# Kernel tuning notes

Measured on AMD Instinct MI355X. Metric: run time of the kernel, lower is better.

## Reference

```python
import jax, jax.numpy as jnp
import numpy as np

H = 256

def setup_inputs() -> dict:
    key = jax.random.key(0)
    ks = jax.random.split(key, 9)
    s = 1.0 / np.sqrt(H)
    x = jax.random.normal(ks[0], (8, 2048, H), dtype=jnp.float32)
    Wq = jax.random.uniform(ks[1], (H, H), jnp.float32, -s, s)
    bq = jax.random.uniform(ks[2], (H,), jnp.float32, -s, s)
    Wk = jax.random.uniform(ks[3], (H, H), jnp.float32, -s, s)
    bk = jax.random.uniform(ks[4], (H,), jnp.float32, -s, s)
    Wv = jax.random.uniform(ks[5], (H, H), jnp.float32, -s, s)
    bv = jax.random.uniform(ks[6], (H,), jnp.float32, -s, s)
    Ww = jax.random.uniform(ks[7], (H, 1), jnp.float32, -s, s)
    bw = jax.random.uniform(ks[8], (1,), jnp.float32, -s, s)
    return {"x": x, "Wq": Wq, "bq": bq, "Wk": Wk, "bk": bk,
            "Wv": Wv, "bv": bv, "Ww": Ww, "bw": bw}

def reference(x, Wq, bq, Wk, bk, Wv, bv, Ww, bw):
    # x: (B, N, H) — cross-asset attention over N assets
    q = x @ Wq + bq
    k = x @ Wk + bk
    v = x @ Wv + bv
    scale = 1.0 / jnp.sqrt(jnp.asarray(q.shape[-1], q.dtype))
    beta = jnp.einsum('bnd,bmd->bnm', q, k) * scale  # (B, N, N)
    beta = jax.nn.softmax(beta, axis=-1)
    # original: sum(value[:,None] * beta[...,None], dim=2) == beta @ v
    out = jnp.einsum('bnm,bmd->bnd', beta, v)
    final_scores = (out @ Ww + bw)[..., 0]  # (B, N)
    return final_scores
```

## Files before the change

kernel.cpp:

```cpp
#include <hip/hip_runtime.h>

#define H 256
#define NB 2048
#define BATCH 8
#define NSPLIT 8
#define KSPAN (NB / NSPLIT)
#define NITER (KSPAN / 64)

typedef unsigned short u16;
using bf16x8 = __attribute__((ext_vector_type(8))) __bf16;
using f32x4  = __attribute__((ext_vector_type(4))) float;

typedef const __attribute__((address_space(1))) void gv_t;
typedef __attribute__((address_space(3))) void lv_t;

__device__ __forceinline__ void gl_lds16(const void* g, void* l) {
    __builtin_amdgcn_global_load_lds((gv_t*)g, (lv_t*)l, 16, 0, 0);
}

#define MFMA(a, b, c) __builtin_amdgcn_mfma_f32_16x16x32_bf16(a, b, c, 0, 0, 0)

__device__ __forceinline__ u16 f2bf(float f) {
    union { float f; unsigned u; } v; v.f = f;
    unsigned r = v.u + 0x7fffu + ((v.u >> 16) & 1u);
    return (u16)(r >> 16);
}

__device__ __forceinline__ bf16x8 cvt8(const float* p) {
    float4 f0 = *(const float4*)p;
    float4 f1 = *(const float4*)(p + 4);
    union { bf16x8 v; u16 u[8]; } r;
    r.u[0] = f2bf(f0.x); r.u[1] = f2bf(f0.y); r.u[2] = f2bf(f0.z); r.u[3] = f2bf(f0.w);
    r.u[4] = f2bf(f1.x); r.u[5] = f2bf(f1.y); r.u[6] = f2bf(f1.z); r.u[7] = f2bf(f1.w);
    return r.v;
}

__global__ __launch_bounds__(256) void prep_kernel(
        const float* __restrict__ Wq, const float* __restrict__ Wk,
        const float* __restrict__ Wv, const float* __restrict__ Ww,
        const float* __restrict__ bq, const float* __restrict__ bv,
        u16* __restrict__ aTb, float* __restrict__ wvw,
        float* __restrict__ kbv, float* __restrict__ ccp, int* __restrict__ cnt) {
    __shared__ u16 bt[16384];
    int id = blockIdx.x, t = threadIdx.x;

    if (id < 256) {
        int f = id;
        if (id == 0 && t < 64) cnt[t] = 0;
        float p = Wv[f * H + t] * Ww[t];
        float r = Wk[f * H + t] * bq[t];
        float c = (id == 0) ? bv[t] * Ww[t] : 0.f;
        for (int o = 32; o; o >>= 1) {
            p += __shfl_xor(p, o); r += __shfl_xor(r, o); c += __shfl_xor(c, o);
        }
        __shared__ float redp[4], redr[4], redc[4];
        int w = t >> 6, lane = t & 63;
        if (lane == 0) { redp[w] = p; redr[w] = r; redc[w] = c; }
        __syncthreads();
        if (t == 0) {
            wvw[f] = redp[0] + redp[1] + redp[2] + redp[3];
            kbv[f] = redr[0] + redr[1] + redr[2] + redr[3];
            if (f == 0) ccp[0] = redc[0] + redc[1] + redc[2] + redc[3];
        }
        return;
    }

    int gid = id - 256;
    int mb = (gid >> 2) * 128, nb = (gid & 3) * 64;
    int w = t >> 6, lane = t & 63, l15 = lane & 15, quad = lane >> 4;

    {
        const float* src = Wq + (nb + w * 16 + l15) * H + quad * 8;
        #pragma unroll
        for (int ks = 0; ks < 8; ++ks)
            *(bf16x8*)(bt + (w * 8 + ks) * 512 + lane * 8) = cvt8(src + ks * 32);
    }

    bf16x8 a[2][8];
    #pragma unroll
    for (int mi = 0; mi < 2; ++mi) {
        const float* ab = Wk + (mb + w * 32 + mi * 16 + l15) * H + quad * 8;
        #pragma unroll
        for (int ks = 0; ks < 8; ++ks) a[mi][ks] = cvt8(ab + ks * 32);
    }
    __syncthreads();

    f32x4 acc[2][4] = {};
    #pragma unroll
    for (int ks = 0; ks < 8; ++ks)
        #pragma unroll
        for (int tt = 0; tt < 4; ++tt) {
            bf16x8 b = *(const bf16x8*)(bt + ((tt * 8 + ks) * 64 + lane) * 8);
            acc[0][tt] = MFMA(a[0][ks], b, acc[0][tt]);
            acc[1][tt] = MFMA(a[1][ks], b, acc[1][tt]);
        }

    #pragma unroll
    for (int mi = 0; mi < 2; ++mi) {
        int m = mb + w * 32 + mi * 16 + quad * 4;
        #pragma unroll
        for (int tt = 0; tt < 4; ++tt) {
            int n = nb + tt * 16 + l15;
            #pragma unroll
            for (int r2 = 0; r2 < 4; ++r2)
                aTb[(m + r2) * H + n] = f2bf(acc[mi][tt][r2] * 0.0625f);
        }
    }
}

__global__ __launch_bounds__(256) void xt_kernel(
        const float* __restrict__ x, const u16* __restrict__ aTb,
        const float* __restrict__ wvw, const float* __restrict__ kbv,
        const float* __restrict__ ccp,
        u16* __restrict__ xbf, float2* __restrict__ uee, u16* __restrict__ Tbf) {
    int id = blockIdx.x, tid = threadIdx.x;
    int w = tid >> 6, lane = tid & 63, l15 = lane & 15, quad = lane >> 4;
    int rb = id * 32;

    bf16x8 a[2][8];
    float s[2] = {0.f, 0.f}, d[2] = {0.f, 0.f};
    #pragma unroll
    for (int ks = 0; ks < 8; ++ks) {
        const float* wp = wvw + ks * 32 + quad * 8;
        const float* kp = kbv + ks * 32 + quad * 8;
        float4 w0 = *(const float4*)wp, w1 = *(const float4*)(wp + 4);
        float4 k0 = *(const float4*)kp, k1 = *(const float4*)(kp + 4);
        #pragma unroll
        for (int mi = 0; mi < 2; ++mi) {
            const float* xr = x + (size_t)(rb + mi * 16 + l15) * H + ks * 32 + quad * 8;
            float4 f0 = *(const float4*)xr;
            float4 f1 = *(const float4*)(xr + 4);
            union { bf16x8 v; u16 u[8]; } r;
            r.u[0] = f2bf(f0.x); r.u[1] = f2bf(f0.y); r.u[2] = f2bf(f0.z); r.u[3] = f2bf(f0.w);
            r.u[4] = f2bf(f1.x); r.u[5] = f2bf(f1.y); r.u[6] = f2bf(f1.z); r.u[7] = f2bf(f1.w);
            a[mi][ks] = r.v;
            s[mi] += f0.x * w0.x + f0.y * w0.y + f0.z * w0.z + f0.w * w0.w
                   + f1.x * w1.x + f1.y * w1.y + f1.z * w1.z + f1.w * w1.w;
            d[mi] += f0.x * k0.x + f0.y * k0.y + f0.z * k0.z + f0.w * k0.w
                   + f1.x * k1.x + f1.y * k1.y + f1.z * k1.z + f1.w * k1.w;
        }
    }

    if (w == 0) {
        #pragma unroll
        for (int mi = 0; mi < 2; ++mi) {
            u16* xo = xbf + (size_t)(rb + mi * 16 + l15) * H + quad * 8;
            #pragma unroll
            for (int ks = 0; ks < 8; ++ks)
                *(bf16x8*)(xo + ks * 32) = a[mi][ks];
        }
        float cc = ccp[0];
        #pragma unroll
        for (int mi = 0; mi < 2; ++mi) {
            float ss = s[mi] + __shfl_xor(s[mi], 16); ss += __shfl_xor(ss, 32);
            float dd = d[mi] + __shfl_xor(d[mi], 16); dd += __shfl_xor(dd, 32);
            if (quad == 0) {
                float e = __expf(dd * 0.0625f);
                uee[rb + mi * 16 + l15] = make_float2(e * (ss + cc), e);
            }
        }
    }

    #pragma unroll 1
    for (int t = 0; t < 4; ++t) {
        int n = (w * 4 + t) * 16 + l15;
        const u16* bb = aTb + n * H + quad * 8;
        bf16x8 bfr[8];
        #pragma unroll
        for (int ks = 0; ks < 8; ++ks) bfr[ks] = *(const bf16x8*)(bb + ks * 32);
        f32x4 acc0 = {}, acc1 = {};
        #pragma unroll
        for (int ks = 0; ks < 8; ++ks) {
            acc0 = MFMA(a[0][ks], bfr[ks], acc0);
            acc1 = MFMA(a[1][ks], bfr[ks], acc1);
        }
        #pragma unroll
        for (int r2 = 0; r2 < 4; ++r2) {
            Tbf[(size_t)(rb + quad * 4 + r2) * H + n]      = f2bf(acc0[r2]);
            Tbf[(size_t)(rb + 16 + quad * 4 + r2) * H + n] = f2bf(acc1[r2]);
        }
    }
}

__global__ __launch_bounds__(256, 2) void attn_kernel(
        const u16* __restrict__ T, const u16* __restrict__ xbf,
        const float2* __restrict__ uee, const float* __restrict__ bw,
        float* __restrict__ pnum, float* __restrict__ pden,
        int* __restrict__ cnt, float* __restrict__ out) {
    __shared__ u16 kt[32768];
    __shared__ int lastf;
    int tid = threadIdx.x;
    int id = blockIdx.x;
    int b = id & 7, rest = id >> 3;
    int qc = rest & 7, sp = rest >> 3;
    int w = tid >> 6, lane = tid & 63, l15 = lane & 15, quad = lane >> 4;
    int qb = qc * 256;

    bf16x8 aq[4][8];
    {
        const u16* qbase = T + (size_t)(b * NB + qb + w * 64 + l15) * H + quad * 8;
        #pragma unroll
        for (int mi = 0; mi < 4; ++mi)
            #pragma unroll
            for (int ks = 0; ks < 8; ++ks)
                aq[mi][ks] = *(const bf16x8*)(qbase + mi * 16 * H + ks * 32);
    }

    const u16* xb = xbf + (size_t)b * NB * H;
    const float2* uep = uee + (size_t)b * NB;
    const int kb0 = sp * KSPAN;

    const u16* gsrc = xb + (size_t)(kb0 + w * 16 + l15) * H + quad * 8;
    #pragma unroll
    for (int j = 0; j < 8; ++j)
        gl_lds16(gsrc + j * 32, kt + (w * 8 + j) * 512);
    __syncthreads();

    float ls[4][4] = {}, as_[4][4] = {};

    #pragma unroll 1
    for (int h = 0; h < NITER; ++h) {
        const u16* ktc = kt + (h & 1) * 16384;
        if (h + 1 < NITER) {
            u16* dst = kt + ((h & 1) ^ 1) * 16384;
            const u16* g2 = gsrc + (size_t)(h + 1) * 64 * H;
            #pragma unroll
            for (int j = 0; j < 8; ++j)
                gl_lds16(g2 + j * 32, dst + (w * 8 + j) * 512);
        }
        int kb64 = kb0 + h * 64;
        float2 uv[4];
        #pragma unroll
        for (int t = 0; t < 4; ++t) uv[t] = uep[kb64 + t * 16 + l15];

        #pragma unroll
        for (int t = 0; t < 4; ++t) {
            f32x4 acc[4] = {};
            __builtin_amdgcn_s_setprio(1);
            #pragma unroll
            for (int ks = 0; ks < 8; ++ks) {
                bf16x8 bfr = *(const bf16x8*)(ktc + ((t * 8 + ks) * 64 + lane) * 8);
                acc[0] = MFMA(aq[0][ks], bfr, acc[0]);
                acc[1] = MFMA(aq[1][ks], bfr, acc[1]);
                acc[2] = MFMA(aq[2][ks], bfr, acc[2]);
                acc[3] = MFMA(aq[3][ks], bfr, acc[3]);
            }
            __builtin_amdgcn_s_setprio(0);
            #pragma unroll
            for (int mi = 0; mi < 4; ++mi)
                #pragma unroll
                for (int r = 0; r < 4; ++r) {
                    float p = __expf(acc[mi][r]);
                    as_[mi][r] += p * uv[t].x;
                    ls[mi][r]  += p * uv[t].y;
                }
        }
        __syncthreads();
    }

    #pragma unroll
    for (int mi = 0; mi < 4; ++mi)
        #pragma unroll
        for (int r = 0; r < 4; ++r)
            for (int o = 1; o < 16; o <<= 1) {
                ls[mi][r]  += __shfl_xor(ls[mi][r], o);
                as_[mi][r] += __shfl_xor(as_[mi][r], o);
            }

    if (l15 == 0) {
        size_t base = (size_t)(sp * BATCH + b) * NB + qb + w * 64 + quad * 4;
        #pragma unroll
        for (int mi = 0; mi < 4; ++mi)
            #pragma unroll
            for (int r = 0; r < 4; ++r) {
                pnum[base + mi * 16 + r] = as_[mi][r];
                pden[base + mi * 16 + r] = ls[mi][r];
            }
    }

    __syncthreads();
    if (tid == 0) {
        __threadfence();
        int old = atomicAdd(cnt + (b * 8 + qc), 1);
        lastf = (old == NSPLIT - 1) ? 1 : 0;
    }
    __syncthreads();
    if (lastf) {
        __threadfence();
        int row = qb + tid;
        float num = 0.f, den = 0.f;
        #pragma unroll
        for (int s2 = 0; s2 < NSPLIT; ++s2) {
            num += pnum[(size_t)(s2 * BATCH + b) * NB + row];
            den += pden[(size_t)(s2 * BATCH + b) * NB + row];
        }
        out[(size_t)b * NB + row] = num / den + bw[0];
    }
}

extern "C" void kernel_launch(void* const* d_in, const int* in_sizes, int n_in,
                              void* d_out, int out_size, void* d_ws, size_t ws_size,
                              hipStream_t stream) {
    (void)in_sizes; (void)n_in; (void)out_size; (void)ws_size;
    const float* x  = (const float*)d_in[0];
    const float* Wq = (const float*)d_in[1];
    const float* bq = (const float*)d_in[2];
    const float* Wk = (const float*)d_in[3];
    const float* bk = (const float*)d_in[4];  (void)bk;
    const float* Wv = (const float*)d_in[5];
    const float* bv = (const float*)d_in[6];
    const float* Ww = (const float*)d_in[7];
    const float* bw = (const float*)d_in[8];
    float* out = (float*)d_out;

    u16* xbf = (u16*)d_ws;
    u16* Tbf = xbf + 4194304;
    u16* aTb = Tbf + 4194304;
    float* wvw = (float*)(aTb + 65536);
    float* kbv = wvw + 256;
    float* ccp = kbv + 256;
    float2* uee = (float2*)(ccp + 4);
    float* pnum = (float*)(uee + 16384);
    float* pden = pnum + NSPLIT * BATCH * NB;
    int* cnt = (int*)(pden + NSPLIT * BATCH * NB);

    hipLaunchKernelGGL(prep_kernel, dim3(264), dim3(256), 0, stream,
                       Wq, Wk, Wv, Ww, bq, bv, aTb, wvw, kbv, ccp, cnt);
    hipLaunchKernelGGL(xt_kernel, dim3(512), dim3(256), 0, stream,
                       x, aTb, wvw, kbv, ccp, xbf, uee, Tbf);
    hipLaunchKernelGGL(attn_kernel, dim3(8 * 8 * NSPLIT), dim3(256), 0, stream,
                       Tbf, xbf, uee, bw, pnum, pden, cnt, out);
}
```

Measured before the change: 147.2 us.

## Use 512-thread attention blocks and move split reduction into a finalize kernel

The attention kernel now runs 8 waves per block, each holding 32 query rows instead of 64. This halves per-wave query registers and accumulators, and each wave loads only half as many key chunks into LDS, so more waves can hide MFMA and exp latency. The atomic-counter last-block reduction is replaced by a separate finalize kernel that sums the split partials. That removes the counter reset and fences but adds one kernel launch, and each wave now reuses every LDS key fragment for fewer MFMAs.

```diff
diff --git a/kernel.cpp b/kernel.cpp
--- a/kernel.cpp
+++ b/kernel.cpp
@@ -40,13 +40,12 @@
         const float* __restrict__ Wv, const float* __restrict__ Ww,
         const float* __restrict__ bq, const float* __restrict__ bv,
         u16* __restrict__ aTb, float* __restrict__ wvw,
-        float* __restrict__ kbv, float* __restrict__ ccp, int* __restrict__ cnt) {
+        float* __restrict__ kbv, float* __restrict__ ccp) {
     __shared__ u16 bt[16384];
     int id = blockIdx.x, t = threadIdx.x;
 
     if (id < 256) {
         int f = id;
-        if (id == 0 && t < 64) cnt[t] = 0;
         float p = Wv[f * H + t] * Ww[t];
         float r = Wk[f * H + t] * bq[t];
         float c = (id == 0) ? bv[t] * Ww[t] : 0.f;
@@ -182,13 +181,11 @@
     }
 }
 
-__global__ __launch_bounds__(256, 2) void attn_kernel(
+__global__ __launch_bounds__(512, 4) void attn_kernel(
         const u16* __restrict__ T, const u16* __restrict__ xbf,
-        const float2* __restrict__ uee, const float* __restrict__ bw,
-        float* __restrict__ pnum, float* __restrict__ pden,
-        int* __restrict__ cnt, float* __restrict__ out) {
+        const float2* __restrict__ uee,
+        float* __restrict__ pnum, float* __restrict__ pden) {
     __shared__ u16 kt[32768];
-    __shared__ int lastf;
     int tid = threadIdx.x;
     int id = blockIdx.x;
     int b = id & 7, rest = id >> 3;
@@ -196,11 +193,11 @@
     int w = tid >> 6, lane = tid & 63, l15 = lane & 15, quad = lane >> 4;
     int qb = qc * 256;
 
-    bf16x8 aq[4][8];
+    bf16x8 aq[2][8];
     {
-        const u16* qbase = T + (size_t)(b * NB + qb + w * 64 + l15) * H + quad * 8;
-        #pragma unroll
-        for (int mi = 0; mi < 4; ++mi)
+        const u16* qbase = T + (size_t)(b * NB + qb + w * 32 + l15) * H + quad * 8;
+        #pragma unroll
+        for (int mi = 0; mi < 2; ++mi)
             #pragma unroll
             for (int ks = 0; ks < 8; ++ks)
                 aq[mi][ks] = *(const bf16x8*)(qbase + mi * 16 * H + ks * 32);
@@ -210,23 +207,28 @@
     const float2* uep = uee + (size_t)b * NB;
     const int kb0 = sp * KSPAN;
 
-    const u16* gsrc = xb + (size_t)(kb0 + w * 16 + l15) * H + quad * 8;
-    #pragma unroll
-    for (int j = 0; j < 8; ++j)
-        gl_lds16(gsrc + j * 32, kt + (w * 8 + j) * 512);
+    #pragma unroll
+    for (int j = 0; j < 4; ++j) {
+        int c = w * 4 + j;
+        gl_lds16(xb + (size_t)(kb0 + (c >> 3) * 16 + l15) * H + (c & 7) * 32 + quad * 8,
+                 kt + c * 512);
+    }
     __syncthreads();
 
-    float ls[4][4] = {}, as_[4][4] = {};
+    float ls[2][4] = {}, as_[2][4] = {};
 
     #pragma unroll 1
     for (int h = 0; h < NITER; ++h) {
         const u16* ktc = kt + (h & 1) * 16384;
         if (h + 1 < NITER) {
+            int kb64n = kb0 + (h + 1) * 64;
             u16* dst = kt + ((h & 1) ^ 1) * 16384;
-            const u16* g2 = gsrc + (size_t)(h + 1) * 64 * H;
-            #pragma unroll
-            for (int j = 0; j < 8; ++j)
-                gl_lds16(g2 + j * 32, dst + (w * 8 + j) * 512);
+            #pragma unroll
+            for (int j = 0; j < 4; ++j) {
+                int c = w * 4 + j;
+                gl_lds16(xb + (size_t)(kb64n + (c >> 3) * 16 + l15) * H + (c & 7) * 32 + quad * 8,
+                         dst + c * 512);
+            }
         }
         int kb64 = kb0 + h * 64;
         float2 uv[4];
@@ -235,31 +237,28 @@
 
         #pragma unroll
         for (int t = 0; t < 4; ++t) {
-            f32x4 acc[4] = {};
+            f32x4 acc0 = {}, acc1 = {};
             __builtin_amdgcn_s_setprio(1);
             #pragma unroll
             for (int ks = 0; ks < 8; ++ks) {
                 bf16x8 bfr = *(const bf16x8*)(ktc + ((t * 8 + ks) * 64 + lane) * 8);
-                acc[0] = MFMA(aq[0][ks], bfr, acc[0]);
-                acc[1] = MFMA(aq[1][ks], bfr, acc[1]);
-                acc[2] = MFMA(aq[2][ks], bfr, acc[2]);
-                acc[3] = MFMA(aq[3][ks], bfr, acc[3]);
+                acc0 = MFMA(aq[0][ks], bfr, acc0);
+                acc1 = MFMA(aq[1][ks], bfr, acc1);
             }
             __builtin_amdgcn_s_setprio(0);
             #pragma unroll
-            for (int mi = 0; mi < 4; ++mi)
-                #pragma unroll
-                for (int r = 0; r < 4; ++r) {
-                    float p = __expf(acc[mi][r]);
-                    as_[mi][r] += p * uv[t].x;
-                    ls[mi][r]  += p * uv[t].y;
-                }
+            for (int r = 0; r < 4; ++r) {
+                float p0 = __expf(acc0[r]);
+                float p1 = __expf(acc1[r]);
+                as_[0][r] += p0 * uv[t].x;  ls[0][r] += p0 * uv[t].y;
+                as_[1][r] += p1 * uv[t].x;  ls[1][r] += p1 * uv[t].y;
+            }
         }
         __syncthreads();
     }
 
     #pragma unroll
-    for (int mi = 0; mi < 4; ++mi)
+    for (int mi = 0; mi < 2; ++mi)
         #pragma unroll
         for (int r = 0; r < 4; ++r)
             for (int o = 1; o < 16; o <<= 1) {
@@ -268,34 +267,27 @@
             }
 
     if (l15 == 0) {
-        size_t base = (size_t)(sp * BATCH + b) * NB + qb + w * 64 + quad * 4;
-        #pragma unroll
-        for (int mi = 0; mi < 4; ++mi)
+        size_t base = (size_t)(sp * BATCH + b) * NB + qb + w * 32 + quad * 4;
+        #pragma unroll
+        for (int mi = 0; mi < 2; ++mi)
             #pragma unroll
             for (int r = 0; r < 4; ++r) {
                 pnum[base + mi * 16 + r] = as_[mi][r];
                 pden[base + mi * 16 + r] = ls[mi][r];
             }
     }
-
-    __syncthreads();
-    if (tid == 0) {
-        __threadfence();
-        int old = atomicAdd(cnt + (b * 8 + qc), 1);
-        lastf = (old == NSPLIT - 1) ? 1 : 0;
-    }
-    __syncthreads();
-    if (lastf) {
-        __threadfence();
-        int row = qb + tid;
-        float num = 0.f, den = 0.f;
-        #pragma unroll
-        for (int s2 = 0; s2 < NSPLIT; ++s2) {
-            num += pnum[(size_t)(s2 * BATCH + b) * NB + row];
-            den += pden[(size_t)(s2 * BATCH + b) * NB + row];
-        }
-        out[(size_t)b * NB + row] = num / den + bw[0];
-    }
+}
+
+__global__ __launch_bounds__(256) void finalize_kernel(
+        const float* __restrict__ pnum, const float* __restrict__ pden,
+        const float* __restrict__ bw, float* __restrict__ out) {
+    int i = blockIdx.x * 256 + threadIdx.x;
+    float num = 0.f, den = 0.f;
+    for (int sp = 0; sp < NSPLIT; ++sp) {
+        num += pnum[sp * (BATCH * NB) + i];
+        den += pden[sp * (BATCH * NB) + i];
+    }
+    out[i] = num / den + bw[0];
 }
 
 extern "C" void kernel_launch(void* const* d_in, const int* in_sizes, int n_in,
@@ -322,12 +314,13 @@
     float2* uee = (float2*)(ccp + 4);
     float* pnum = (float*)(uee + 16384);
     float* pden = pnum + NSPLIT * BATCH * NB;
-    int* cnt = (int*)(pden + NSPLIT * BATCH * NB);
 
     hipLaunchKernelGGL(prep_kernel, dim3(264), dim3(256), 0, stream,
-                       Wq, Wk, Wv, Ww, bq, bv, aTb, wvw, kbv, ccp, cnt);
+                       Wq, Wk, Wv, Ww, bq, bv, aTb, wvw, kbv, ccp);
     hipLaunchKernelGGL(xt_kernel, dim3(512), dim3(256), 0, stream,
                        x, aTb, wvw, kbv, ccp, xbf, uee, Tbf);
-    hipLaunchKernelGGL(attn_kernel, dim3(8 * 8 * NSPLIT), dim3(256), 0, stream,
-                       Tbf, xbf, uee, bw, pnum, pden, cnt, out);
-}
+    hipLaunchKernelGGL(attn_kernel, dim3(8 * 8 * NSPLIT), dim3(512), 0, stream,
+                       Tbf, xbf, uee, pnum, pden);
+    hipLaunchKernelGGL(finalize_kernel, dim3(64), dim3(256), 0, stream,
+                       pnum, pden, bw, out);
+}
```

New measurement: 139.3 us. -5.4%, faster.
